# Performance work log

Hardware: AMD Instinct MI355X
Metric: run time of the kernel (lower is better)

The kernel has to match this reference:

```python
import jax, jax.numpy as jnp
import numpy as np

B, C = 2, 4
SPATIAL = (128, 128, 128)
N_PTS = 32          # num_points_per_class
THR = 0.5           # threshold


def setup_inputs() -> dict:
    key = jax.random.key(0)
    logits = jax.random.normal(key, (B, C) + SPATIAL, dtype=jnp.float32)
    return {"logits": logits}


def _extract_points(logits):
    """Vectorized equivalent of the per-(batch,class) nonzero/topk loop.

    For every (b, c): softmax prob > THR defines candidates; top-k by prob
    selects up to N_PTS points. Classes are visited in the original order
    (foreground 1..C-1, then background 0); valid points are compacted to
    the front per batch element; padding has label -1 and coords 0.
    Output width is fixed at C*N_PTS (jit-friendly) instead of the batch
    max count, but all valid (coord, label) entries and their order match.
    """
    b, c = logits.shape[:2]
    spatial = logits.shape[2:]
    dims = len(spatial)
    S = int(np.prod(spatial))
    probs = jax.nn.softmax(logits, axis=1).reshape(b, c, S)  # [b,c,S]
    # class visitation order: 1..C-1 then 0 (background last)
    order = jnp.concatenate([jnp.arange(1, c), jnp.arange(1)])  # [c]
    probs = probs[:, order]                                    # [b,c,S]
    score = jnp.where(probs > THR, probs, -jnp.inf)
    top_vals, top_idx = jax.lax.top_k(score, N_PTS)            # [b,c,N_PTS]
    valid = top_vals > -jnp.inf                                # [b,c,N_PTS]
    coords = jnp.stack(jnp.unravel_index(top_idx, spatial), axis=-1)  # [b,c,N_PTS,dims]
    labels = jnp.where(valid, order[None, :, None], -1)        # [b,c,N_PTS]
    coords = jnp.where(valid[..., None], coords, 0)
    # flatten classes and compact valid points to the front (stable sort)
    N = c * N_PTS
    labels = labels.reshape(b, N)
    coords = coords.reshape(b, N, dims)
    perm = jnp.argsort((labels < 0).astype(jnp.int32), axis=1, stable=True)  # [b,N]
    labels = jnp.take_along_axis(labels, perm, axis=1)
    coords = jnp.take_along_axis(coords, perm[..., None], axis=1)
    return coords.astype(jnp.int32), labels.astype(jnp.int32)


def reference(logits):
    coords, labels = _extract_points(logits)
    return coords, labels
```

## Files before the change

### kernel.cpp

```cpp
#include <hip/hip_runtime.h>
#include <stdint.h>

#define Bn 2
#define Cn 4
#define Sn (128 * 128 * 128)
#define NPTS 32
#define NBINS 1025
#define THRf 0.5f
#define PB 4096
#define BT 512
#define BT2 1024
#define FB 1024

__device__ __forceinline__ int bin_of_bits(unsigned int u) {
    return (int)((u - 0x3F000000u) >> 13);
}

__device__ __forceinline__ void softmax_argmax4(float l0, float l1, float l2, float l3,
                                                int* cm_out, float* p_out) {
    float m = fmaxf(fmaxf(l0, l1), fmaxf(l2, l3));
    float e0 = expf(l0 - m);
    float e1 = expf(l1 - m);
    float e2 = expf(l2 - m);
    float e3 = expf(l3 - m);
    float s = ((e0 + e1) + e2) + e3;
    float em = e0; int cm = 0;
    if (e1 > em) { em = e1; cm = 1; }
    if (e2 > em) { em = e2; cm = 2; }
    if (e3 > em) { em = e3; cm = 3; }
    *cm_out = cm;
    *p_out = em / s;
}


__global__ __launch_bounds__(BT) void fused_stream(const float* __restrict__ logits,
                                                   unsigned int* __restrict__ cnt,
                                                   unsigned int* __restrict__ gh,
                                                   uint2* __restrict__ cand,
                                                   int cap) {
    __shared__ unsigned int lh[Cn * NBINS];
    __shared__ unsigned int lcut[Cn], cls_cnt[Cn], cls_base[Cn], cls_pos[Cn];
    const int b = blockIdx.y;
    const int t = threadIdx.x;
    const int lane = t & 63;
    for (int j = t; j < Cn * NBINS; j += BT) lh[j] = 0u;
    if (t < Cn) { lcut[t] = 0u; cls_cnt[t] = 0u; cls_pos[t] = 0u; }
    __syncthreads();

    const float* base = logits + (size_t)b * Cn * Sn;
    const float4* s0 = (const float4*)base;
    const float4* s1 = (const float4*)(base + Sn);
    const float4* s2 = (const float4*)(base + 2 * Sn);
    const float4* s3 = (const float4*)(base + 3 * Sn);
    const int qs = blockIdx.x * (PB / 4);
    unsigned int pk[PB / BT];
    #pragma unroll
    for (int it = 0; it < PB / 4 / BT; ++it) {
        int q = qs + it * BT + t;
        float4 v0 = s0[q], v1 = s1[q], v2 = s2[q], v3 = s3[q];
        const float* a0 = &v0.x; const float* a1 = &v1.x;
        const float* a2 = &v2.x; const float* a3 = &v3.x;
        #pragma unroll
        for (int k = 0; k < 4; ++k) {
            int cm; float p;
            softmax_argmax4(a0[k], a1[k], a2[k], a3[k], &cm, &p);
            unsigned int pv = 0u;
            if (p > THRf) {
                unsigned int off = __float_as_uint(p) - 0x3F000000u;
                atomicAdd(&lh[cm * NBINS + (int)(off >> 13)], 1u);
                pv = (off << 2) | (unsigned int)cm;
            }
            pk[it * 4 + k] = pv;
        }
    }
    __syncthreads();

    {
        const int wave = t >> 6;
        if (wave < Cn) {
            const unsigned int* h = &lh[wave * NBINS];
            const int lo = lane * 17;
            unsigned int cs = 0;
            #pragma unroll
            for (int k = 0; k < 17; ++k) {
                int bin = lo + k;
                if (bin < NBINS) cs += h[bin];
            }
            unsigned int S = cs;
            #pragma unroll
            for (int off = 1; off < 64; off <<= 1) {
                unsigned int v = __shfl_down(S, off, 64);
                if (lane + off < 64) S += v;
            }
            unsigned int suf = S - cs;
            if (S >= NPTS && suf < NPTS) {
                unsigned int acc = suf;
                int hi = min(lo + 16, NBINS - 1);
                for (int bin = hi; bin >= lo; --bin) {
                    acc += h[bin];
                    if (acc >= NPTS) {
                        lcut[wave] = (unsigned int)bin;
                        cls_cnt[wave] = acc;
                        break;
                    }
                }
            }
            if (lane == 0 && S < NPTS) cls_cnt[wave] = S;
        }
    }
    __syncthreads();

    {
        const int wave = t >> 6;
        if (wave < Cn) {
            const unsigned int* h = &lh[wave * NBINS];
            unsigned int* g = gh + (size_t)(b * Cn + wave) * NBINS;
            for (int bin = (int)lcut[wave] + lane; bin < NBINS; bin += 64) {
                unsigned int v = h[bin];
                if (v) atomicAdd(&g[bin], v);
            }
        }
    }
    if (t < Cn && cls_cnt[t] > 0)
        cls_base[t] = atomicAdd(&cnt[b * Cn + t], cls_cnt[t]);
    __syncthreads();

    #pragma unroll
    for (int j = 0; j < PB / BT; ++j) {
        unsigned int pv = pk[j];
        if (pv != 0u) {
            unsigned int cm = pv & 3u;
            if ((pv >> 15) >= lcut[cm]) {
                unsigned int pos = cls_base[cm] + atomicAdd(&cls_pos[cm], 1u);
                if (pos < (unsigned int)cap) {
                    int it = j >> 2, k = j & 3;
                    unsigned int idx = (unsigned int)((qs + it * BT + t) * 4 + k);
                    cand[(size_t)(b * Cn + cm) * cap + pos] =
                        make_uint2(0x3F000000u + (pv >> 2), idx);
                }
            }
        }
    }
}

__global__ __launch_bounds__(BT2) void select_emit(const unsigned int* __restrict__ cnt,
                                                   const unsigned int* __restrict__ gh,
                                                   const uint2* __restrict__ cand,
                                                   int cap,
                                                   unsigned int* __restrict__ done,
                                                   unsigned int* __restrict__ validn,
                                                   uint2* __restrict__ topk,
                                                   int* __restrict__ out) {
    __shared__ unsigned int lh[NBINS];
    __shared__ uint2 fbuf[FB];
    __shared__ unsigned int s_T, s_m, s_old;
    __shared__ int pre[Cn + 1];
    const int bc = blockIdx.x, t = threadIdx.x;
    const int b = bc >> 2;
    const int lane = t & 63;

    for (int j = t; j < NBINS; j += BT2) lh[j] = gh[(size_t)bc * NBINS + j];
    if (t == 0) { s_T = 0u; s_m = 0u; }
    __syncthreads();
    const int n = min((int)cnt[bc], cap);

    if (t < 64) {
        const int lo = lane * 17;
        unsigned int cs = 0;
        #pragma unroll
        for (int k = 0; k < 17; ++k) {
            int bin = lo + k;
            if (bin < NBINS) cs += lh[bin];
        }
        unsigned int S = cs;
        #pragma unroll
        for (int off = 1; off < 64; off <<= 1) {
            unsigned int v = __shfl_down(S, off, 64);
            if (lane + off < 64) S += v;
        }
        unsigned int suf = S - cs;
        if (S >= NPTS && suf < NPTS) {
            unsigned int acc = suf;
            int hi = min(lo + 16, NBINS - 1);
            for (int bin = hi; bin >= lo; --bin) {
                acc += lh[bin];
                if (acc >= NPTS) { s_T = (unsigned int)bin; break; }
            }
        }
    }
    __syncthreads();
    const unsigned int T = s_T;

    {
        const uint2* src = cand + (size_t)bc * cap;
        for (int j0 = t; j0 < n; j0 += BT2 * 8) {
            uint2 e[8];
            #pragma unroll
            for (int k = 0; k < 8; ++k) {
                int j = j0 + k * BT2;
                e[k] = src[j < n ? j : (n > 0 ? n - 1 : 0)];
            }
            #pragma unroll
            for (int k = 0; k < 8; ++k) {
                int j = j0 + k * BT2;
                if (j < n && (unsigned int)bin_of_bits(e[k].x) >= T) {
                    unsigned int pos = atomicAdd(&s_m, 1u);
                    if (pos < FB) fbuf[pos] = e[k];
                }
            }
        }
    }
    __syncthreads();

    const int m = min((int)s_m, FB);
    const int vn = min(n, NPTS);
    if (t == 0) validn[bc] = (unsigned int)vn;
    for (int i = t; i < m; i += BT2) {
        uint2 e = fbuf[i];
        int rank = 0;
        for (int j = 0; j < m; ++j) {
            uint2 o = fbuf[j];
            rank += (int)((o.x > e.x) || (o.x == e.x && o.y < e.y));
        }
        if (rank < vn) topk[bc * NPTS + rank] = e;
    }

    __threadfence();
    __syncthreads();
    if (t == 0) s_old = atomicAdd(&done[b], 1u);
    __syncthreads();
    if (s_old != 3u) return;
    __threadfence();

    if (t == 0) {
        int acc = 0;
        for (int oc = 0; oc < Cn; ++oc) {
            pre[oc] = acc;
            acc += (int)validn[b * Cn + ((oc + 1) & 3)];
        }
        pre[Cn] = acc;
    }
    __syncthreads();

    if (t < Cn * NPTS) {
        const int j = t;
        int label = -1, z = 0, y = 0, x = 0;
        if (j < pre[Cn]) {
            int oc = 0;
            while (j >= pre[oc + 1]) ++oc;
            int c = (oc + 1) & 3;
            int r = j - pre[oc];
            uint2 e = topk[(b * Cn + c) * NPTS + r];
            int idx = (int)e.y;
            z = idx >> 14;
            y = (idx >> 7) & 127;
            x = idx & 127;
            label = c;
        }
        int* coords = out;
        int* labels = out + Bn * Cn * NPTS * 3;
        int bo = b * Cn * NPTS + j;
        coords[bo * 3 + 0] = z;
        coords[bo * 3 + 1] = y;
        coords[bo * 3 + 2] = x;
        labels[bo] = label;
    }
}

extern "C" void kernel_launch(void* const* d_in, const int* in_sizes, int n_in,
                              void* d_out, int out_size, void* d_ws, size_t ws_size,
                              hipStream_t stream) {
    const float* logits = (const float*)d_in[0];
    int* out = (int*)d_out;

    unsigned int* cnt = (unsigned int*)d_ws;
    unsigned int* done = cnt + Bn * Cn;
    unsigned int* gh = done + Bn;
    unsigned int* validn = gh + Bn * Cn * NBINS;
    uint2* topk = (uint2*)(validn + Bn * Cn);
    uint2* cand = topk + Bn * Cn * NPTS;
    size_t fixed = (size_t)((char*)cand - (char*)d_ws);
    int cap = (int)((ws_size - fixed) / (Bn * Cn * sizeof(uint2)));
    if (cap > (1 << 18)) cap = 1 << 18;
    if (cap < 4096) cap = 4096;

    hipMemsetAsync(cnt, 0, (size_t)(Bn * Cn + Bn + Bn * Cn * NBINS) * sizeof(unsigned int),
                   stream);

    dim3 grid(Sn / PB, Bn);
    fused_stream<<<grid, BT, 0, stream>>>(logits, cnt, gh, cand, cap);
    select_emit<<<Bn * Cn, BT2, 0, stream>>>(cnt, gh, cand, cap, done, validn, topk, out);
}
```

Measured before the change: 117.8 us.

## Prefilter candidates with fast exp sum and queue them in LDS for exact pass

The streaming pass now computes only a cheap softmax denominator with __expf and flags elements whose exp-sum is below about 2, which is a necessary condition for the max probability to exceed 0.5. Flagged local indices are compacted into an LDS queue using a wave ballot, mbcnt and one atomic per wave. A second loop reloads those elements and runs the exact softmax/argmax, histogram and candidate packing. This removes the per-thread packed register array and the full softmax work on rejected elements, at the cost of re-reading flagged logits and a fixed queue capacity. Candidates past that capacity are silently dropped, which risks wrong results on inputs with many confident points.

```diff
diff --git a/kernel.cpp b/kernel.cpp
--- a/kernel.cpp
+++ b/kernel.cpp
@@ -11,6 +11,9 @@
 #define BT 512
 #define BT2 1024
 #define FB 1024
+#define QCAP 3072
+
+typedef float f32x4 __attribute__((ext_vector_type(4)));
 
 __device__ __forceinline__ int bin_of_bits(unsigned int u) {
     return (int)((u - 0x3F000000u) >> 13);
@@ -39,39 +42,63 @@
                                                    uint2* __restrict__ cand,
                                                    int cap) {
     __shared__ unsigned int lh[Cn * NBINS];
+    __shared__ unsigned short qidx[QCAP];
+    __shared__ unsigned int qpv[QCAP];
     __shared__ unsigned int lcut[Cn], cls_cnt[Cn], cls_base[Cn], cls_pos[Cn];
+    __shared__ unsigned int qn;
     const int b = blockIdx.y;
     const int t = threadIdx.x;
     const int lane = t & 63;
     for (int j = t; j < Cn * NBINS; j += BT) lh[j] = 0u;
     if (t < Cn) { lcut[t] = 0u; cls_cnt[t] = 0u; cls_pos[t] = 0u; }
+    if (t == 0) qn = 0u;
     __syncthreads();
 
     const float* base = logits + (size_t)b * Cn * Sn;
-    const float4* s0 = (const float4*)base;
-    const float4* s1 = (const float4*)(base + Sn);
-    const float4* s2 = (const float4*)(base + 2 * Sn);
-    const float4* s3 = (const float4*)(base + 3 * Sn);
+    const f32x4* s0 = (const f32x4*)base;
+    const f32x4* s1 = (const f32x4*)(base + Sn);
+    const f32x4* s2 = (const f32x4*)(base + 2 * Sn);
+    const f32x4* s3 = (const f32x4*)(base + 3 * Sn);
     const int qs = blockIdx.x * (PB / 4);
-    unsigned int pk[PB / BT];
+
     #pragma unroll
     for (int it = 0; it < PB / 4 / BT; ++it) {
         int q = qs + it * BT + t;
-        float4 v0 = s0[q], v1 = s1[q], v2 = s2[q], v3 = s3[q];
-        const float* a0 = &v0.x; const float* a1 = &v1.x;
-        const float* a2 = &v2.x; const float* a3 = &v3.x;
+        f32x4 v0 = s0[q], v1 = s1[q], v2 = s2[q], v3 = s3[q];
         #pragma unroll
         for (int k = 0; k < 4; ++k) {
-            int cm; float p;
-            softmax_argmax4(a0[k], a1[k], a2[k], a3[k], &cm, &p);
-            unsigned int pv = 0u;
-            if (p > THRf) {
-                unsigned int off = __float_as_uint(p) - 0x3F000000u;
-                atomicAdd(&lh[cm * NBINS + (int)(off >> 13)], 1u);
-                pv = (off << 2) | (unsigned int)cm;
-            }
-            pk[it * 4 + k] = pv;
-        }
+            float l0 = v0[k], l1 = v1[k], l2 = v2[k], l3 = v3[k];
+            float m = fmaxf(fmaxf(l0, l1), fmaxf(l2, l3));
+            float st = ((__expf(l0 - m) + __expf(l1 - m)) + __expf(l2 - m)) + __expf(l3 - m);
+            bool c = st < 2.001f;
+            unsigned long long mk = __ballot(c);
+            unsigned int wb = 0u;
+            unsigned int nset = (unsigned int)__popcll(mk);
+            if (lane == 0 && nset) wb = atomicAdd(&qn, nset);
+            wb = __shfl(wb, 0);
+            unsigned int pos = wb + __builtin_amdgcn_mbcnt_hi(
+                (unsigned int)(mk >> 32),
+                __builtin_amdgcn_mbcnt_lo((unsigned int)mk, 0u));
+            if (c && pos < QCAP)
+                qidx[pos] = (unsigned short)((it * BT + t) * 4 + k);
+        }
+    }
+    __syncthreads();
+
+    const int nq = min((int)qn, QCAP);
+    for (int i = t; i < nq; i += BT) {
+        int lv = qidx[i];
+        int gv = (qs << 2) + lv;
+        float l0 = base[gv], l1 = base[Sn + gv], l2 = base[2 * Sn + gv], l3 = base[3 * Sn + gv];
+        int cm; float p;
+        softmax_argmax4(l0, l1, l2, l3, &cm, &p);
+        unsigned int pv = 0u;
+        if (p > THRf) {
+            unsigned int off = __float_as_uint(p) - 0x3F000000u;
+            atomicAdd(&lh[cm * NBINS + (int)(off >> 13)], 1u);
+            pv = (off << 2) | (unsigned int)cm;
+        }
+        qpv[i] = pv;
     }
     __syncthreads();
 
@@ -125,16 +152,14 @@
         cls_base[t] = atomicAdd(&cnt[b * Cn + t], cls_cnt[t]);
     __syncthreads();
 
-    #pragma unroll
-    for (int j = 0; j < PB / BT; ++j) {
-        unsigned int pv = pk[j];
+    for (int i = t; i < nq; i += BT) {
+        unsigned int pv = qpv[i];
         if (pv != 0u) {
             unsigned int cm = pv & 3u;
             if ((pv >> 15) >= lcut[cm]) {
                 unsigned int pos = cls_base[cm] + atomicAdd(&cls_pos[cm], 1u);
                 if (pos < (unsigned int)cap) {
-                    int it = j >> 2, k = j & 3;
-                    unsigned int idx = (unsigned int)((qs + it * BT + t) * 4 + k);
+                    unsigned int idx = (unsigned int)((qs << 2) + qidx[i]);
                     cand[(size_t)(b * Cn + cm) * cap + pos] =
                         make_uint2(0x3F000000u + (pv >> 2), idx);
                 }
```

Measured after the change: 132.0 us. 12.1% more time.
